# Performance work log

Measured on AMD Instinct MI355X. Metric: run time of the kernel, lower is better.

## Reference

```python
import jax, jax.numpy as jnp
import numpy as np

F, V, E = 26, 100000, 16          # fields, vocab per field, embedding dim
CONT, H1, H2 = 13, 400, 400
B = 16384


def setup_inputs() -> dict:
    key = jax.random.key(0)
    ks = jax.random.split(key, 12)
    dnn_in_dim = CONT + F * E  # 429
    return {
        "continuous": jax.random.normal(ks[0], (B, CONT), jnp.float32),
        "categorical": jax.random.randint(ks[1], (B, F), 0, V, jnp.int32),
        "w_cont": jax.random.normal(ks[2], (CONT, 1), jnp.float32) * 0.05,
        "b_cont": jnp.zeros((1,), jnp.float32),
        "tables_first": jax.random.normal(ks[3], (F, V, 1), jnp.float32) * 0.05,
        "tables_emb": jax.random.normal(ks[4], (F, V, E), jnp.float32) * 0.05,
        "W1": jax.random.normal(ks[5], (dnn_in_dim, H1), jnp.float32) * 0.05,
        "b1": jnp.zeros((H1,), jnp.float32),
        "W2": jax.random.normal(ks[6], (H1, H2), jnp.float32) * 0.05,
        "b2": jnp.zeros((H2,), jnp.float32),
        "W_out": jax.random.normal(ks[7], (H2 + 1, 1), jnp.float32) * 0.05,
        "b_out": jnp.zeros((1,), jnp.float32),
    }


def reference(continuous, categorical, w_cont, b_cont, tables_first, tables_emb,
              W1, b1, W2, b2, W_out, b_out):
    # per-field gather: tables [F,V,D], categorical [B,F] -> [B,F,D]
    gather = jax.vmap(lambda tab, idx: tab[idx], in_axes=(0, 1), out_axes=1)
    # ---- FM first order ----
    first = gather(tables_first, categorical)            # [B, F, 1]
    fm1 = continuous @ w_cont + b_cont + jnp.sum(first, axis=1)  # [B, 1]
    # ---- FM second order (sum-square trick) ----
    emb = gather(tables_emb, categorical)                # [B, F, E]
    sum_emb = jnp.sum(emb, axis=1)                       # [B, E]
    sum_square = jnp.sum(jnp.square(emb), axis=1)        # [B, E]
    fm2 = 0.5 * jnp.sum(jnp.square(sum_emb) - sum_square, axis=1, keepdims=True)
    fm_out = fm1 + fm2                                   # [B, 1]
    # ---- DNN (dropout is identity at inference) ----
    dnn_in = jnp.concatenate([continuous, emb.reshape(emb.shape[0], -1)], axis=1)
    h = jax.nn.relu(dnn_in @ W1 + b1)
    h = jax.nn.relu(h @ W2 + b2)
    fusion = jnp.concatenate([fm_out, h], axis=1)        # [B, 1+H2]
    return fusion @ W_out + b_out                        # [B, 1]
```

## Files before the change

### kernel.cpp

```cpp
#include <hip/hip_runtime.h>

typedef unsigned short ushort_t;
typedef unsigned int uint_t;

__device__ __forceinline__ float bf2f(ushort_t u) {
    union { float f; uint_t i; } c; c.i = ((uint_t)u) << 16; return c.f;
}
__device__ __forceinline__ ushort_t f2bf(float f) {
    union { float f; uint_t i; } c; c.f = f;
    uint_t i = c.i;
    uint_t r = (i + 0x7fffu + ((i >> 16) & 1u)) >> 16;
    return (ushort_t)r;
}

typedef __attribute__((ext_vector_type(8))) short short8;
typedef __attribute__((ext_vector_type(4))) float float4v;

#define BATCH 16384
#define NF    26
#define NV    100000
#define ED    16
#define NCONT 13
#define H     400
#define K1    480
#define K2    416

#define OFF_DNN   0u
#define OFF_A2    15728640u
#define OFF_W1T   29360128u
#define OFF_W2T   29744128u
#define OFF_FM    30076928u
#define OFF_OACC  30142464u

__global__ void prep_weights(const float* __restrict__ W1,
                             const float* __restrict__ W2,
                             ushort_t* __restrict__ W1t,
                             ushort_t* __restrict__ W2t) {
    int i = blockIdx.x * 256 + threadIdx.x;
    if (i < H * K1) {
        int n = i / K1, k = i % K1;
        ushort_t o = 0;
        if (k < 416) {
            o = f2bf(W1[(size_t)(13 + k) * H + n]);
        } else if (k < 448) {
            int j = k - (k < 432 ? 416 : 432);
            if (j < NCONT) o = f2bf(W1[(size_t)j * H + n]);
        } else if (k < 464) {
            int j = k - 448;
            if (j < NCONT) {
                float w = W1[(size_t)j * H + n];
                ushort_t wh = f2bf(w);
                o = f2bf(w - bf2f(wh));
            }
        }
        W1t[i] = o;
    } else {
        int j = i - H * K1;
        if (j < H * K2) {
            int n = j / K2, k = j % K2;
            W2t[j] = (k < 400) ? f2bf(W2[(size_t)k * H + n]) : (ushort_t)0;
        }
    }
}

__global__ __launch_bounds__(256) void gather_fm(
    const float* __restrict__ cont, const int* __restrict__ cat,
    const float* __restrict__ w_cont, const float* __restrict__ b_cont,
    const float* __restrict__ t_first, const float* __restrict__ t_emb,
    ushort_t* __restrict__ dnn, ushort_t* __restrict__ A2,
    float* __restrict__ fm_out) {
    int tid  = threadIdx.x;
    int lane = tid & 63;
    int b    = blockIdx.x * 4 + (tid >> 6);

    int idxv = (lane < NF) ? cat[b * NF + lane] : 0;

    float p = 0.f;
    if (lane < NCONT) {
        float c = cont[b * NCONT + lane];
        ushort_t ch = f2bf(c);
        float cl = c - bf2f(ch);
        dnn[(size_t)b * K1 + 416 + lane] = ch;
        dnn[(size_t)b * K1 + 432 + lane] = f2bf(cl);
        dnn[(size_t)b * K1 + 448 + lane] = ch;
        p = c * w_cont[lane];
    } else if (lane < 16) {
        dnn[(size_t)b * K1 + 416 + lane] = 0;
        dnn[(size_t)b * K1 + 432 + lane] = 0;
        dnn[(size_t)b * K1 + 448 + lane] = 0;
    }
    if (lane < 16) dnn[(size_t)b * K1 + 464 + lane] = 0;
    if (lane < NF) p += t_first[(size_t)lane * NV + idxv];
    #pragma unroll
    for (int off = 1; off < 64; off <<= 1) p += __shfl_xor(p, off);

    int e = lane & 15, fsub = lane >> 4;
    float s = 0.f, ss = 0.f;
    for (int it = 0; it < 7; ++it) {
        int f = it * 4 + fsub;
        if (f < NF) {
            int idxf = __shfl(idxv, f);
            float v = t_emb[((size_t)(f * NV + idxf)) * ED + e];
            dnn[(size_t)b * K1 + f * ED + e] = f2bf(v);
            s += v; ss += v * v;
        }
    }
    s  += __shfl_xor(s, 16);  s  += __shfl_xor(s, 32);
    ss += __shfl_xor(ss, 16); ss += __shfl_xor(ss, 32);
    float u = s * s - ss;
    u += __shfl_xor(u, 1); u += __shfl_xor(u, 2);
    u += __shfl_xor(u, 4); u += __shfl_xor(u, 8);

    if (lane == 0) fm_out[b] = p + b_cont[0] + 0.5f * u;

    if (lane < 16) A2[(size_t)b * K2 + 400 + lane] = 0;
}

__global__ __launch_bounds__(256) void gemm1_k(
    const ushort_t* __restrict__ A, const ushort_t* __restrict__ Bt,
    const float* __restrict__ bias, ushort_t* __restrict__ A2) {
    __shared__ __align__(16) ushort_t lsa[128 * 40];
    __shared__ __align__(16) ushort_t lsb[80 * 40];
    int tid  = threadIdx.x;
    int m0   = (blockIdx.x / 5) * 128;
    int n0   = (blockIdx.x % 5) * 80;
    int wave = tid >> 6, lane = tid & 63;
    int quad = lane >> 4, mrow = lane & 15;

    float4v acc[2][5] = {};

    for (int k0 = 0; k0 < K1; k0 += 32) {
        __syncthreads();
        #pragma unroll
        for (int c = tid; c < 512; c += 256) {
            int r = c >> 2, sgm = c & 3;
            *(uint4*)(&lsa[r * 40 + sgm * 8]) =
                *(const uint4*)(&A[(size_t)(m0 + r) * K1 + k0 + sgm * 8]);
        }
        for (int c = tid; c < 320; c += 256) {
            int r = c >> 2, sgm = c & 3;
            *(uint4*)(&lsb[r * 40 + sgm * 8]) =
                *(const uint4*)(&Bt[(size_t)(n0 + r) * K1 + k0 + sgm * 8]);
        }
        __syncthreads();
        short8 af0 = *(const short8*)(&lsa[(wave * 32 + mrow) * 40 + quad * 8]);
        short8 af1 = *(const short8*)(&lsa[(wave * 32 + 16 + mrow) * 40 + quad * 8]);
        #pragma unroll
        for (int ni = 0; ni < 5; ++ni) {
            short8 bfr = *(const short8*)(&lsb[(ni * 16 + mrow) * 40 + quad * 8]);
            acc[0][ni] = __builtin_amdgcn_mfma_f32_16x16x32_bf16(af0, bfr, acc[0][ni], 0, 0, 0);
            acc[1][ni] = __builtin_amdgcn_mfma_f32_16x16x32_bf16(af1, bfr, acc[1][ni], 0, 0, 0);
        }
    }

    #pragma unroll
    for (int mi = 0; mi < 2; ++mi)
        #pragma unroll
        for (int ni = 0; ni < 5; ++ni) {
            int col = n0 + ni * 16 + mrow;
            float bv = bias[col];
            #pragma unroll
            for (int reg = 0; reg < 4; ++reg) {
                int row = m0 + wave * 32 + mi * 16 + quad * 4 + reg;
                float h = fmaxf(acc[mi][ni][reg] + bv, 0.f);
                A2[(size_t)row * K2 + col] = f2bf(h);
            }
        }
}

__global__ __launch_bounds__(256) void gemm2_k(
    const ushort_t* __restrict__ A, const ushort_t* __restrict__ Bt,
    const float* __restrict__ bias, const float* __restrict__ Wout,
    float* __restrict__ oacc) {
    __shared__ __align__(16) ushort_t lsa[128 * 40];
    __shared__ __align__(16) ushort_t lsb[80 * 40];
    int tid  = threadIdx.x;
    int m0   = (blockIdx.x / 5) * 128;
    int n0   = (blockIdx.x % 5) * 80;
    int wave = tid >> 6, lane = tid & 63;
    int quad = lane >> 4, mrow = lane & 15;

    float4v acc[2][5] = {};

    for (int k0 = 0; k0 < K2; k0 += 32) {
        __syncthreads();
        #pragma unroll
        for (int c = tid; c < 512; c += 256) {
            int r = c >> 2, sgm = c & 3;
            *(uint4*)(&lsa[r * 40 + sgm * 8]) =
                *(const uint4*)(&A[(size_t)(m0 + r) * K2 + k0 + sgm * 8]);
        }
        for (int c = tid; c < 320; c += 256) {
            int r = c >> 2, sgm = c & 3;
            *(uint4*)(&lsb[r * 40 + sgm * 8]) =
                *(const uint4*)(&Bt[(size_t)(n0 + r) * K2 + k0 + sgm * 8]);
        }
        __syncthreads();
        short8 af0 = *(const short8*)(&lsa[(wave * 32 + mrow) * 40 + quad * 8]);
        short8 af1 = *(const short8*)(&lsa[(wave * 32 + 16 + mrow) * 40 + quad * 8]);
        #pragma unroll
        for (int ni = 0; ni < 5; ++ni) {
            short8 bfr = *(const short8*)(&lsb[(ni * 16 + mrow) * 40 + quad * 8]);
            acc[0][ni] = __builtin_amdgcn_mfma_f32_16x16x32_bf16(af0, bfr, acc[0][ni], 0, 0, 0);
            acc[1][ni] = __builtin_amdgcn_mfma_f32_16x16x32_bf16(af1, bfr, acc[1][ni], 0, 0, 0);
        }
    }

    float p0[4] = {0.f, 0.f, 0.f, 0.f};
    float p1[4] = {0.f, 0.f, 0.f, 0.f};
    #pragma unroll
    for (int ni = 0; ni < 5; ++ni) {
        int col = n0 + ni * 16 + mrow;
        float bv = bias[col];
        float wv = Wout[1 + col];
        #pragma unroll
        for (int reg = 0; reg < 4; ++reg) {
            p0[reg] += fmaxf(acc[0][ni][reg] + bv, 0.f) * wv;
            p1[reg] += fmaxf(acc[1][ni][reg] + bv, 0.f) * wv;
        }
    }
    #pragma unroll
    for (int reg = 0; reg < 4; ++reg) {
        #pragma unroll
        for (int off = 1; off < 16; off <<= 1) {
            p0[reg] += __shfl_xor(p0[reg], off);
            p1[reg] += __shfl_xor(p1[reg], off);
        }
    }
    if (mrow == 0) {
        int rbase = m0 + wave * 32 + quad * 4;
        #pragma unroll
        for (int reg = 0; reg < 4; ++reg) {
            atomicAdd(&oacc[rbase + reg],      p0[reg]);
            atomicAdd(&oacc[rbase + 16 + reg], p1[reg]);
        }
    }
}

__global__ void finalize_k(const float* __restrict__ oacc,
                           const float* __restrict__ fm_out,
                           const float* __restrict__ Wout,
                           const float* __restrict__ bout,
                           float* __restrict__ out) {
    int i = blockIdx.x * 256 + threadIdx.x;
    out[i] = oacc[i] + fm_out[i] * Wout[0] + bout[0];
}

extern "C" void kernel_launch(void* const* d_in, const int* in_sizes, int n_in,
                              void* d_out, int out_size, void* d_ws, size_t ws_size,
                              hipStream_t stream) {
    const float* cont    = (const float*)d_in[0];
    const int*   cat     = (const int*)d_in[1];
    const float* w_cont  = (const float*)d_in[2];
    const float* b_cont  = (const float*)d_in[3];
    const float* t_first = (const float*)d_in[4];
    const float* t_emb   = (const float*)d_in[5];
    const float* W1      = (const float*)d_in[6];
    const float* b1      = (const float*)d_in[7];
    const float* W2      = (const float*)d_in[8];
    const float* b2      = (const float*)d_in[9];
    const float* Wout    = (const float*)d_in[10];
    const float* bout    = (const float*)d_in[11];
    float* out = (float*)d_out;

    char* w = (char*)d_ws;
    ushort_t* dnn  = (ushort_t*)(w + OFF_DNN);
    ushort_t* A2   = (ushort_t*)(w + OFF_A2);
    ushort_t* W1t  = (ushort_t*)(w + OFF_W1T);
    ushort_t* W2t  = (ushort_t*)(w + OFF_W2T);
    float*    fm   = (float*)(w + OFF_FM);
    float*    oacc = (float*)(w + OFF_OACC);

    prep_weights<<<1400, 256, 0, stream>>>(W1, W2, W1t, W2t);
    gather_fm<<<BATCH / 4, 256, 0, stream>>>(cont, cat, w_cont, b_cont,
                                             t_first, t_emb, dnn, A2, fm);
    hipMemsetAsync(oacc, 0, BATCH * sizeof(float), stream);
    gemm1_k<<<(BATCH / 128) * 5, 256, 0, stream>>>(dnn, W1t, b1, A2);
    gemm2_k<<<(BATCH / 128) * 5, 256, 0, stream>>>(A2, W2t, b2, Wout, oacc);
    finalize_k<<<BATCH / 256, 256, 0, stream>>>(oacc, fm, Wout, bout, out);
}
```

Before: 301.9 us.

## Fuse gather, both MLP GEMMs and output into one per-64-row kernel

Replaces the gather, two GEMM kernels, memset and finalize with a single kernel. Each block gathers embeddings for 64 rows into LDS, runs layer 1 from LDS with weights streamed from global into registers, writes the hidden activations back into the same LDS buffer, runs layer 2 and reduces the output in-block. Weight rows are padded to 448 so four waves split the N dimension evenly. This removes the HBM round trips for the dnn input and hidden activations, the atomics and several launches. In exchange, B fragments are reloaded from global/L2 by every block with no LDS sharing, and the large LDS tile plus 28 accumulators per wave limit occupancy.

```diff
diff --git a/kernel.cpp b/kernel.cpp
--- a/kernel.cpp
+++ b/kernel.cpp
@@ -9,241 +9,222 @@
 __device__ __forceinline__ ushort_t f2bf(float f) {
     union { float f; uint_t i; } c; c.f = f;
     uint_t i = c.i;
-    uint_t r = (i + 0x7fffu + ((i >> 16) & 1u)) >> 16;
-    return (ushort_t)r;
+    return (ushort_t)((i + 0x7fffu + ((i >> 16) & 1u)) >> 16);
 }
 
 typedef __attribute__((ext_vector_type(8))) short short8;
 typedef __attribute__((ext_vector_type(4))) float float4v;
 
 #define BATCH 16384
-#define NF    26
 #define NV    100000
-#define ED    16
-#define NCONT 13
-#define H     400
+#define NPAD  448
 #define K1    480
 #define K2    416
-
-#define OFF_DNN   0u
-#define OFF_A2    15728640u
-#define OFF_W1T   29360128u
-#define OFF_W2T   29744128u
-#define OFF_FM    30076928u
-#define OFF_OACC  30142464u
-
-__global__ void prep_weights(const float* __restrict__ W1,
-                             const float* __restrict__ W2,
-                             ushort_t* __restrict__ W1t,
-                             ushort_t* __restrict__ W2t) {
+#define SA    488
+#define SH    456
+
+#define OFF_W1T 0u
+#define OFF_W2T 430080u
+
+__global__ void prep_weights(const float* __restrict__ W1, const float* __restrict__ W2,
+                             ushort_t* __restrict__ W1t, ushort_t* __restrict__ W2t) {
     int i = blockIdx.x * 256 + threadIdx.x;
-    if (i < H * K1) {
+    if (i < NPAD * K1) {
         int n = i / K1, k = i % K1;
         ushort_t o = 0;
-        if (k < 416) {
-            o = f2bf(W1[(size_t)(13 + k) * H + n]);
-        } else if (k < 448) {
-            int j = k - (k < 432 ? 416 : 432);
-            if (j < NCONT) o = f2bf(W1[(size_t)j * H + n]);
-        } else if (k < 464) {
-            int j = k - 448;
-            if (j < NCONT) {
-                float w = W1[(size_t)j * H + n];
-                ushort_t wh = f2bf(w);
-                o = f2bf(w - bf2f(wh));
+        if (n < 400) {
+            if (k < 416) {
+                o = f2bf(W1[(size_t)(13 + k) * 400 + n]);
+            } else if (k < 448) {
+                int j = k - (k < 432 ? 416 : 432);
+                if (j < 13) o = f2bf(W1[(size_t)j * 400 + n]);
+            } else if (k < 464) {
+                int j = k - 448;
+                if (j < 13) {
+                    float wv = W1[(size_t)j * 400 + n];
+                    ushort_t wh = f2bf(wv);
+                    o = f2bf(wv - bf2f(wh));
+                }
             }
         }
         W1t[i] = o;
     } else {
-        int j = i - H * K1;
-        if (j < H * K2) {
+        int j = i - NPAD * K1;
+        if (j < NPAD * K2) {
             int n = j / K2, k = j % K2;
-            W2t[j] = (k < 400) ? f2bf(W2[(size_t)k * H + n]) : (ushort_t)0;
-        }
-    }
-}
-
-__global__ __launch_bounds__(256) void gather_fm(
+            W2t[j] = (n < 400 && k < 400) ? f2bf(W2[(size_t)k * 400 + n]) : (ushort_t)0;
+        }
+    }
+}
+
+__global__ __launch_bounds__(256, 2) void fused_deepfm(
     const float* __restrict__ cont, const int* __restrict__ cat,
     const float* __restrict__ w_cont, const float* __restrict__ b_cont,
     const float* __restrict__ t_first, const float* __restrict__ t_emb,
-    ushort_t* __restrict__ dnn, ushort_t* __restrict__ A2,
-    float* __restrict__ fm_out) {
+    const ushort_t* __restrict__ W1t, const float* __restrict__ b1,
+    const ushort_t* __restrict__ W2t, const float* __restrict__ b2,
+    const float* __restrict__ Wout, const float* __restrict__ bout,
+    float* __restrict__ out)
+{
+    __shared__ __align__(16) ushort_t smA[64 * SA];
+    __shared__ float smFM[64];
+    __shared__ float smP[256];
+
     int tid  = threadIdx.x;
-    int lane = tid & 63;
-    int b    = blockIdx.x * 4 + (tid >> 6);
-
-    int idxv = (lane < NF) ? cat[b * NF + lane] : 0;
-
-    float p = 0.f;
-    if (lane < NCONT) {
-        float c = cont[b * NCONT + lane];
-        ushort_t ch = f2bf(c);
-        float cl = c - bf2f(ch);
-        dnn[(size_t)b * K1 + 416 + lane] = ch;
-        dnn[(size_t)b * K1 + 432 + lane] = f2bf(cl);
-        dnn[(size_t)b * K1 + 448 + lane] = ch;
-        p = c * w_cont[lane];
-    } else if (lane < 16) {
-        dnn[(size_t)b * K1 + 416 + lane] = 0;
-        dnn[(size_t)b * K1 + 432 + lane] = 0;
-        dnn[(size_t)b * K1 + 448 + lane] = 0;
-    }
-    if (lane < 16) dnn[(size_t)b * K1 + 464 + lane] = 0;
-    if (lane < NF) p += t_first[(size_t)lane * NV + idxv];
-    #pragma unroll
-    for (int off = 1; off < 64; off <<= 1) p += __shfl_xor(p, off);
-
-    int e = lane & 15, fsub = lane >> 4;
-    float s = 0.f, ss = 0.f;
-    for (int it = 0; it < 7; ++it) {
-        int f = it * 4 + fsub;
-        if (f < NF) {
-            int idxf = __shfl(idxv, f);
-            float v = t_emb[((size_t)(f * NV + idxf)) * ED + e];
-            dnn[(size_t)b * K1 + f * ED + e] = f2bf(v);
-            s += v; ss += v * v;
-        }
-    }
-    s  += __shfl_xor(s, 16);  s  += __shfl_xor(s, 32);
-    ss += __shfl_xor(ss, 16); ss += __shfl_xor(ss, 32);
-    float u = s * s - ss;
-    u += __shfl_xor(u, 1); u += __shfl_xor(u, 2);
-    u += __shfl_xor(u, 4); u += __shfl_xor(u, 8);
-
-    if (lane == 0) fm_out[b] = p + b_cont[0] + 0.5f * u;
-
-    if (lane < 16) A2[(size_t)b * K2 + 400 + lane] = 0;
-}
-
-__global__ __launch_bounds__(256) void gemm1_k(
-    const ushort_t* __restrict__ A, const ushort_t* __restrict__ Bt,
-    const float* __restrict__ bias, ushort_t* __restrict__ A2) {
-    __shared__ __align__(16) ushort_t lsa[128 * 40];
-    __shared__ __align__(16) ushort_t lsb[80 * 40];
-    int tid  = threadIdx.x;
-    int m0   = (blockIdx.x / 5) * 128;
-    int n0   = (blockIdx.x % 5) * 80;
-    int wave = tid >> 6, lane = tid & 63;
+    int wv   = tid >> 6, lane = tid & 63;
     int quad = lane >> 4, mrow = lane & 15;
-
-    float4v acc[2][5] = {};
-
-    for (int k0 = 0; k0 < K1; k0 += 32) {
+    int b0   = blockIdx.x * 64;
+    ushort_t* smH = smA;
+
+    {
+        int r4 = lane >> 4, fs = (lane >> 2) & 3, sub = lane & 3, l16 = lane & 15;
+        for (int g = 0; g < 4; ++g) {
+            int R  = wv * 16 + g * 4 + r4;
+            int gR = b0 + R;
+            float sj0 = 0, sj1 = 0, sj2 = 0, sj3 = 0, ssq = 0, pacc = 0;
+            #pragma unroll
+            for (int it = 0; it < 7; ++it) {
+                int f = it * 4 + fs;
+                if (f < 26) {
+                    int idx = cat[gR * 26 + f];
+                    const float* ep = t_emb + (((size_t)f * NV + idx) << 4) + sub * 4;
+                    float4 v = *(const float4*)ep;
+                    sj0 += v.x; sj1 += v.y; sj2 += v.z; sj3 += v.w;
+                    ssq += v.x * v.x + v.y * v.y + v.z * v.z + v.w * v.w;
+                    uint_t lo = (uint_t)f2bf(v.x) | ((uint_t)f2bf(v.y) << 16);
+                    uint_t hi = (uint_t)f2bf(v.z) | ((uint_t)f2bf(v.w) << 16);
+                    uint2 pk = make_uint2(lo, hi);
+                    *(uint2*)&smA[R * SA + f * 16 + sub * 4] = pk;
+                    if (sub == 0) pacc += t_first[(size_t)f * NV + idx];
+                }
+            }
+            float c = (l16 < 13) ? cont[gR * 13 + l16] : 0.f;
+            if (l16 < 13) pacc += c * w_cont[l16];
+            ushort_t ch = f2bf(c);
+            float cl = c - bf2f(ch);
+            smA[R * SA + 416 + l16] = ch;
+            smA[R * SA + 432 + l16] = f2bf(cl);
+            smA[R * SA + 448 + l16] = ch;
+            smA[R * SA + 464 + l16] = 0;
+            sj0 += __shfl_xor(sj0, 4); sj0 += __shfl_xor(sj0, 8);
+            sj1 += __shfl_xor(sj1, 4); sj1 += __shfl_xor(sj1, 8);
+            sj2 += __shfl_xor(sj2, 4); sj2 += __shfl_xor(sj2, 8);
+            sj3 += __shfl_xor(sj3, 4); sj3 += __shfl_xor(sj3, 8);
+            float q = pacc - 0.5f * ssq;
+            if (fs == 0) q += 0.5f * (sj0 * sj0 + sj1 * sj1 + sj2 * sj2 + sj3 * sj3);
+            q += __shfl_xor(q, 1); q += __shfl_xor(q, 2);
+            q += __shfl_xor(q, 4); q += __shfl_xor(q, 8);
+            if (l16 == 0) smFM[R] = q + b_cont[0];
+        }
+    }
+    __syncthreads();
+
+    int n0 = wv * 7;
+
+    {
+        const ushort_t* Bb = W1t + (size_t)mrow * K1 + quad * 8;
+        short8 bcur[7], bnxt[7];
+        #pragma unroll
+        for (int ni = 0; ni < 7; ++ni)
+            bcur[ni] = *(const short8*)(Bb + (size_t)(n0 + ni) * 16 * K1);
+        float4v acc[4][7] = {};
+        #pragma unroll 1
+        for (int s = 0; s < 15; ++s) {
+            if (s < 14) {
+                #pragma unroll
+                for (int ni = 0; ni < 7; ++ni)
+                    bnxt[ni] = *(const short8*)(Bb + (size_t)(n0 + ni) * 16 * K1 + (s + 1) * 32);
+            }
+            short8 af[4];
+            #pragma unroll
+            for (int mt = 0; mt < 4; ++mt)
+                af[mt] = *(const short8*)&smA[(mt * 16 + mrow) * SA + s * 32 + quad * 8];
+            #pragma unroll
+            for (int ni = 0; ni < 7; ++ni)
+                #pragma unroll
+                for (int mt = 0; mt < 4; ++mt)
+                    acc[mt][ni] = __builtin_amdgcn_mfma_f32_16x16x32_bf16(af[mt], bcur[ni], acc[mt][ni], 0, 0, 0);
+            #pragma unroll
+            for (int ni = 0; ni < 7; ++ni) bcur[ni] = bnxt[ni];
+        }
         __syncthreads();
         #pragma unroll
-        for (int c = tid; c < 512; c += 256) {
-            int r = c >> 2, sgm = c & 3;
-            *(uint4*)(&lsa[r * 40 + sgm * 8]) =
-                *(const uint4*)(&A[(size_t)(m0 + r) * K1 + k0 + sgm * 8]);
-        }
-        for (int c = tid; c < 320; c += 256) {
-            int r = c >> 2, sgm = c & 3;
-            *(uint4*)(&lsb[r * 40 + sgm * 8]) =
-                *(const uint4*)(&Bt[(size_t)(n0 + r) * K1 + k0 + sgm * 8]);
-        }
-        __syncthreads();
-        short8 af0 = *(const short8*)(&lsa[(wave * 32 + mrow) * 40 + quad * 8]);
-        short8 af1 = *(const short8*)(&lsa[(wave * 32 + 16 + mrow) * 40 + quad * 8]);
-        #pragma unroll
-        for (int ni = 0; ni < 5; ++ni) {
-            short8 bfr = *(const short8*)(&lsb[(ni * 16 + mrow) * 40 + quad * 8]);
-            acc[0][ni] = __builtin_amdgcn_mfma_f32_16x16x32_bf16(af0, bfr, acc[0][ni], 0, 0, 0);
-            acc[1][ni] = __builtin_amdgcn_mfma_f32_16x16x32_bf16(af1, bfr, acc[1][ni], 0, 0, 0);
-        }
-    }
-
-    #pragma unroll
-    for (int mi = 0; mi < 2; ++mi)
-        #pragma unroll
-        for (int ni = 0; ni < 5; ++ni) {
-            int col = n0 + ni * 16 + mrow;
-            float bv = bias[col];
-            #pragma unroll
-            for (int reg = 0; reg < 4; ++reg) {
-                int row = m0 + wave * 32 + mi * 16 + quad * 4 + reg;
-                float h = fmaxf(acc[mi][ni][reg] + bv, 0.f);
-                A2[(size_t)row * K2 + col] = f2bf(h);
-            }
-        }
-}
-
-__global__ __launch_bounds__(256) void gemm2_k(
-    const ushort_t* __restrict__ A, const ushort_t* __restrict__ Bt,
-    const float* __restrict__ bias, const float* __restrict__ Wout,
-    float* __restrict__ oacc) {
-    __shared__ __align__(16) ushort_t lsa[128 * 40];
-    __shared__ __align__(16) ushort_t lsb[80 * 40];
-    int tid  = threadIdx.x;
-    int m0   = (blockIdx.x / 5) * 128;
-    int n0   = (blockIdx.x % 5) * 80;
-    int wave = tid >> 6, lane = tid & 63;
-    int quad = lane >> 4, mrow = lane & 15;
-
-    float4v acc[2][5] = {};
-
-    for (int k0 = 0; k0 < K2; k0 += 32) {
-        __syncthreads();
-        #pragma unroll
-        for (int c = tid; c < 512; c += 256) {
-            int r = c >> 2, sgm = c & 3;
-            *(uint4*)(&lsa[r * 40 + sgm * 8]) =
-                *(const uint4*)(&A[(size_t)(m0 + r) * K2 + k0 + sgm * 8]);
-        }
-        for (int c = tid; c < 320; c += 256) {
-            int r = c >> 2, sgm = c & 3;
-            *(uint4*)(&lsb[r * 40 + sgm * 8]) =
-                *(const uint4*)(&Bt[(size_t)(n0 + r) * K2 + k0 + sgm * 8]);
-        }
-        __syncthreads();
-        short8 af0 = *(const short8*)(&lsa[(wave * 32 + mrow) * 40 + quad * 8]);
-        short8 af1 = *(const short8*)(&lsa[(wave * 32 + 16 + mrow) * 40 + quad * 8]);
-        #pragma unroll
-        for (int ni = 0; ni < 5; ++ni) {
-            short8 bfr = *(const short8*)(&lsb[(ni * 16 + mrow) * 40 + quad * 8]);
-            acc[0][ni] = __builtin_amdgcn_mfma_f32_16x16x32_bf16(af0, bfr, acc[0][ni], 0, 0, 0);
-            acc[1][ni] = __builtin_amdgcn_mfma_f32_16x16x32_bf16(af1, bfr, acc[1][ni], 0, 0, 0);
-        }
-    }
-
-    float p0[4] = {0.f, 0.f, 0.f, 0.f};
-    float p1[4] = {0.f, 0.f, 0.f, 0.f};
-    #pragma unroll
-    for (int ni = 0; ni < 5; ++ni) {
-        int col = n0 + ni * 16 + mrow;
-        float bv = bias[col];
-        float wv = Wout[1 + col];
-        #pragma unroll
-        for (int reg = 0; reg < 4; ++reg) {
-            p0[reg] += fmaxf(acc[0][ni][reg] + bv, 0.f) * wv;
-            p1[reg] += fmaxf(acc[1][ni][reg] + bv, 0.f) * wv;
-        }
-    }
-    #pragma unroll
-    for (int reg = 0; reg < 4; ++reg) {
-        #pragma unroll
-        for (int off = 1; off < 16; off <<= 1) {
-            p0[reg] += __shfl_xor(p0[reg], off);
-            p1[reg] += __shfl_xor(p1[reg], off);
-        }
-    }
-    if (mrow == 0) {
-        int rbase = m0 + wave * 32 + quad * 4;
-        #pragma unroll
-        for (int reg = 0; reg < 4; ++reg) {
-            atomicAdd(&oacc[rbase + reg],      p0[reg]);
-            atomicAdd(&oacc[rbase + 16 + reg], p1[reg]);
-        }
-    }
-}
-
-__global__ void finalize_k(const float* __restrict__ oacc,
-                           const float* __restrict__ fm_out,
-                           const float* __restrict__ Wout,
-                           const float* __restrict__ bout,
-                           float* __restrict__ out) {
-    int i = blockIdx.x * 256 + threadIdx.x;
-    out[i] = oacc[i] + fm_out[i] * Wout[0] + bout[0];
+        for (int ni = 0; ni < 7; ++ni) {
+            int col = n0 * 16 + ni * 16 + mrow;
+            float bv = (col < 400) ? b1[col] : 0.f;
+            #pragma unroll
+            for (int mt = 0; mt < 4; ++mt)
+                #pragma unroll
+                for (int r = 0; r < 4; ++r) {
+                    int row = mt * 16 + quad * 4 + r;
+                    smH[row * SH + col] = f2bf(fmaxf(acc[mt][ni][r] + bv, 0.f));
+                }
+        }
+    }
+    __syncthreads();
+
+    {
+        const ushort_t* Bb = W2t + (size_t)mrow * K2 + quad * 8;
+        short8 bcur[7], bnxt[7];
+        #pragma unroll
+        for (int ni = 0; ni < 7; ++ni)
+            bcur[ni] = *(const short8*)(Bb + (size_t)(n0 + ni) * 16 * K2);
+        float4v acc[4][7] = {};
+        #pragma unroll 1
+        for (int s = 0; s < 13; ++s) {
+            if (s < 12) {
+                #pragma unroll
+                for (int ni = 0; ni < 7; ++ni)
+                    bnxt[ni] = *(const short8*)(Bb + (size_t)(n0 + ni) * 16 * K2 + (s + 1) * 32);
+            }
+            short8 af[4];
+            #pragma unroll
+            for (int mt = 0; mt < 4; ++mt)
+                af[mt] = *(const short8*)&smH[(mt * 16 + mrow) * SH + s * 32 + quad * 8];
+            #pragma unroll
+            for (int ni = 0; ni < 7; ++ni)
+                #pragma unroll
+                for (int mt = 0; mt < 4; ++mt)
+                    acc[mt][ni] = __builtin_amdgcn_mfma_f32_16x16x32_bf16(af[mt], bcur[ni], acc[mt][ni], 0, 0, 0);
+            #pragma unroll
+            for (int ni = 0; ni < 7; ++ni) bcur[ni] = bnxt[ni];
+        }
+        float p[4][4] = {};
+        #pragma unroll
+        for (int ni = 0; ni < 7; ++ni) {
+            int col = n0 * 16 + ni * 16 + mrow;
+            if (col < 400) {
+                float bv = b2[col], wvv = Wout[1 + col];
+                #pragma unroll
+                for (int mt = 0; mt < 4; ++mt)
+                    #pragma unroll
+                    for (int r = 0; r < 4; ++r)
+                        p[mt][r] += fmaxf(acc[mt][ni][r] + bv, 0.f) * wvv;
+            }
+        }
+        #pragma unroll
+        for (int mt = 0; mt < 4; ++mt)
+            #pragma unroll
+            for (int r = 0; r < 4; ++r) {
+                float v = p[mt][r];
+                v += __shfl_xor(v, 1); v += __shfl_xor(v, 2);
+                v += __shfl_xor(v, 4); v += __shfl_xor(v, 8);
+                p[mt][r] = v;
+            }
+        if (mrow == 0) {
+            #pragma unroll
+            for (int mt = 0; mt < 4; ++mt)
+                #pragma unroll
+                for (int r = 0; r < 4; ++r)
+                    smP[wv * 64 + mt * 16 + quad * 4 + r] = p[mt][r];
+        }
+    }
+    __syncthreads();
+
+    if (tid < 64) {
+        float o = smP[tid] + smP[64 + tid] + smP[128 + tid] + smP[192 + tid];
+        out[b0 + tid] = o + smFM[tid] * Wout[0] + bout[0];
+    }
 }
 
 extern "C" void kernel_launch(void* const* d_in, const int* in_sizes, int n_in,
@@ -264,18 +245,11 @@
     float* out = (float*)d_out;
 
     char* w = (char*)d_ws;
-    ushort_t* dnn  = (ushort_t*)(w + OFF_DNN);
-    ushort_t* A2   = (ushort_t*)(w + OFF_A2);
-    ushort_t* W1t  = (ushort_t*)(w + OFF_W1T);
-    ushort_t* W2t  = (ushort_t*)(w + OFF_W2T);
-    float*    fm   = (float*)(w + OFF_FM);
-    float*    oacc = (float*)(w + OFF_OACC);
-
-    prep_weights<<<1400, 256, 0, stream>>>(W1, W2, W1t, W2t);
-    gather_fm<<<BATCH / 4, 256, 0, stream>>>(cont, cat, w_cont, b_cont,
-                                             t_first, t_emb, dnn, A2, fm);
-    hipMemsetAsync(oacc, 0, BATCH * sizeof(float), stream);
-    gemm1_k<<<(BATCH / 128) * 5, 256, 0, stream>>>(dnn, W1t, b1, A2);
-    gemm2_k<<<(BATCH / 128) * 5, 256, 0, stream>>>(A2, W2t, b2, Wout, oacc);
-    finalize_k<<<BATCH / 256, 256, 0, stream>>>(oacc, fm, Wout, bout, out);
-}
+    ushort_t* W1t = (ushort_t*)(w + OFF_W1T);
+    ushort_t* W2t = (ushort_t*)(w + OFF_W2T);
+
+    prep_weights<<<1568, 256, 0, stream>>>(W1, W2, W1t, W2t);
+    fused_deepfm<<<BATCH / 64, 256, 0, stream>>>(cont, cat, w_cont, b_cont,
+                                                 t_first, t_emb, W1t, b1, W2t, b2,
+                                                 Wout, bout, out);
+}
```

New measurement: 284.8 us. 1.06x faster.
